# Performance work log

Hardware: AMD Instinct MI355X
Metric: run time of the kernel (lower is better)

The kernel has to match this reference:

```python
import jax, jax.numpy as jnp
import numpy as np

NUM_ITERATIONS = 5
BIG = 1e30


def _compute_cv(vc, Hf, norm):
    # vc: [B, M, N]; Hf: [M, N] float 0/1 mask; norm: scalar normalization factor
    # sign part: product of signs of incoming messages per check, redistributed
    sign_info = (1.0 - Hf)[None] + vc            # non-edges -> +1 so they don't affect the product
    s = jnp.sign(sign_info)
    row_sign = jnp.prod(s, axis=2, keepdims=True)  # [B, M, 1]
    result_sign = row_sign * Hf * s              # extrinsic sign per edge (self sign divided out)
    # magnitude part: min / second-min over edges of each check (masked top-2)
    back = jnp.where(Hf == 0.0, -BIG - 1.0, 0.0)[None]  # push non-edges to -inf-ish
    a = jnp.clip(jnp.abs(vc), 0.0, BIG)
    decision = -a + back                          # top-2 of this = two smallest magnitudes on edges
    top2 = jax.lax.top_k(decision, 2)[0]          # [B, M, 2]
    mn = (-top2[:, :, 0:1]) * Hf                  # smallest magnitude, broadcast on edges
    sub = (-top2[:, :, 1:2]) * Hf                 # second smallest
    res = jnp.where(a > mn, mn, sub)              # extrinsic min (exclude self if self is the min)
    return norm * res * jax.lax.stop_gradient(result_sign)


def setup_inputs() -> dict:
    key = jax.random.key(0)
    k1, k2, k3 = jax.random.split(key, 3)
    B, M, N = 16, 1024, 2048
    soft_input = jax.random.normal(k1, (B, N), dtype=jnp.float32) * 2.0
    # sparse binary parity-check matrix (Tanner graph), ~20 ones per row, min degree 2
    H = (jax.random.uniform(k2, (M, N)) < 0.01).astype(jnp.int32)
    H = H.at[:, :2].set(1)
    labels = jax.random.randint(k3, (B, N), 0, 2).astype(jnp.int32)
    w = jnp.full((1,), -0.048, dtype=jnp.float32)
    return {"soft_input": soft_input, "H": H, "labels": labels, "w": w}


def reference(soft_input, H, labels, w):
    Hf = H.astype(jnp.float32)
    norm = jax.nn.softplus(w)  # NMS-1 normalized factor, shape [1]
    soft_output = soft_input
    for _ in range(NUM_ITERATIONS):
        vc = soft_output[:, None, :] * Hf          # variable-to-check messages [B, M, N]
        cv = _compute_cv(vc, Hf, norm)             # check-to-variable messages [B, M, N]
        soft_output = soft_input + jnp.sum(cv, axis=1)  # marginalize
    return soft_output
```

## Files before the change

kernel.cpp:

```cpp
#include <hip/hip_runtime.h>

#define BB 16
#define MM 1024
#define NN 2048
#define RCAP 64
#define CCAP 48
#define INFF __builtin_inff()

typedef unsigned short u16;

__device__ __forceinline__ float signf(float x) {
    return (x > 0.0f) ? 1.0f : ((x < 0.0f) ? -1.0f : 0.0f);
}

__device__ __forceinline__ void mmerge(float& mn, float& sub, float om, float os) {
    float hi = fmaxf(mn, om);
    mn = fminf(mn, om);
    sub = fminf(fminf(sub, os), hi);
}

__global__ __launch_bounds__(256)
void build_stats1(const int4* __restrict__ H4, const float* __restrict__ soft_in,
                  int* __restrict__ row_deg, u16* __restrict__ row_cols,
                  int* __restrict__ col_deg, u16* __restrict__ col_rows,
                  float4* __restrict__ stats_out, const float* __restrict__ wptr) {
    __shared__ u16 s_cols[RCAP];
    __shared__ int s_cnt;
    const int m = blockIdx.x, t = threadIdx.x;
    if (t == 0) s_cnt = 0;
    __syncthreads();

    const int4* hrow = H4 + m * (NN / 4);
#pragma unroll
    for (int half = 0; half < 2; ++half) {
        int i = t + half * 256;
        int4 h = hrow[i];
        int hv[4] = {h.x, h.y, h.z, h.w};
#pragma unroll
        for (int k = 0; k < 4; ++k) {
            if (hv[k]) {
                int c = i * 4 + k;
                int j = atomicAdd(&s_cnt, 1);
                if (j < RCAP) s_cols[j] = (u16)c;
                if (c >= 2) {
                    int j2 = atomicAdd(&col_deg[c], 1);
                    if (j2 < CCAP) col_rows[c * CCAP + j2] = (u16)m;
                }
            }
        }
    }
    __syncthreads();
    const int deg = min(s_cnt, RCAP);
    if (t == 0) row_deg[m] = deg;
    if (t < 8) ((int4*)(row_cols + m * RCAP))[t] = ((const int4*)s_cols)[t];

    const int b = t >> 4, k = t & 15;
    const float norm = log1pf(expf(wptr[0]));
    const float* sp = soft_in + b * NN;
    float sgn = 1.0f, mn = INFF, sub = INFF;
    for (int j = k; j < deg; j += 16) {
        float x = sp[s_cols[j]];
        sgn *= signf(x);
        float a = fabsf(x);
        if (a < mn) { sub = mn; mn = a; }
        else if (a < sub) sub = a;
    }
#pragma unroll
    for (int off = 1; off < 16; off <<= 1) {
        sgn *= __shfl_xor(sgn, off, 16);
        float om = __shfl_xor(mn, off, 16);
        float os = __shfl_xor(sub, off, 16);
        mmerge(mn, sub, om, os);
    }
    if (k == 0) stats_out[b * MM + m] = make_float4(norm * sgn, mn, sub, 0.0f);
}

__global__ __launch_bounds__(64)
void phase_a(const float* __restrict__ soft,
             const int* __restrict__ row_deg, const u16* __restrict__ row_cols,
             float4* __restrict__ stats_out, const float* __restrict__ wptr) {
    const int blk = blockIdx.x;
    const int b = blk >> 4;
    const int m = ((blk & 15) << 6) + threadIdx.x;
    const float norm = log1pf(expf(wptr[0]));
    const float* sp = soft + b * NN;
    const int deg = row_deg[m];
    const int4* ip = (const int4*)(row_cols + m * RCAP);
    float sgn = 1.0f, mn = INFF, sub = INFF;
#pragma unroll
    for (int jb = 0; jb < RCAP; jb += 8) {
        if (jb < deg) {
            int4 iv = ip[jb >> 3];
            const u16* q = (const u16*)&iv;
#pragma unroll
            for (int k = 0; k < 8; ++k) {
                float x = sp[q[k] & (NN - 1)];
                x = (jb + k < deg) ? x : INFF;
                sgn *= signf(x);
                float a = fabsf(x);
                if (a < mn) { sub = mn; mn = a; }
                else if (a < sub) sub = a;
            }
        }
    }
    stats_out[b * MM + m] = make_float4(norm * sgn, mn, sub, 0.0f);
}

__global__ __launch_bounds__(64)
void phase_b(const float* __restrict__ soft_src, const float* __restrict__ soft_in,
             float* __restrict__ dst, const float4* __restrict__ stats,
             const int* __restrict__ col_deg, const u16* __restrict__ col_rows) {
    const int blk = blockIdx.x, t = threadIdx.x;
    if (blk < 512) {
        const int b = blk >> 5;
        const int n = ((blk & 31) << 6) + t;
        if (n < 2) return;
        const float4* st = stats + b * MM;
        float x = soft_src[b * NN + n];
        float a = fabsf(x), sx = signf(x), acc = 0.0f;
        const int deg = min(col_deg[n], CCAP);
        const int4* ip = (const int4*)(col_rows + n * CCAP);
#pragma unroll
        for (int jb = 0; jb < CCAP; jb += 8) {
            if (jb < deg) {
                int4 iv = ip[jb >> 3];
                const u16* q = (const u16*)&iv;
#pragma unroll
                for (int k = 0; k < 8; ++k) {
                    float4 s = st[q[k] & (MM - 1)];
                    float cv = s.x * ((a > s.y) ? s.y : s.z) * sx;
                    acc += (jb + k < deg) ? cv : 0.0f;
                }
            }
        }
        dst[b * NN + n] = soft_in[b * NN + n] + acc;
    } else {
        const int h = blk - 512;
        const int b = h >> 1, c = h & 1;
        const float4* st = stats + b * MM;
        float x = soft_src[b * NN + c];
        float a = fabsf(x), sx = signf(x), acc = 0.0f;
#pragma unroll
        for (int i = 0; i < 16; ++i) {
            float4 s = st[t + 64 * i];
            acc += s.x * ((a > s.y) ? s.y : s.z) * sx;
        }
#pragma unroll
        for (int off = 1; off < 64; off <<= 1) acc += __shfl_xor(acc, off);
        if (t == 0) dst[b * NN + c] = soft_in[b * NN + c] + acc;
    }
}

extern "C" void kernel_launch(void* const* d_in, const int* in_sizes, int n_in,
                              void* d_out, int out_size, void* d_ws, size_t ws_size,
                              hipStream_t stream) {
    const float* soft_in = (const float*)d_in[0];
    const int*   H       = (const int*)d_in[1];
    const float* w       = (const float*)d_in[3];
    float* out = (float*)d_out;

    char* ws = (char*)d_ws;
    int* col_deg  = (int*)ws;
    int* row_deg  = (int*)(ws + 8192);
    u16* row_cols = (u16*)(ws + 12288);
    u16* col_rows = (u16*)(ws + 143360);
    float4* statsA = (float4*)(ws + 339968);
    float4* statsB = (float4*)(ws + 602112);
    float* softX = (float*)(ws + 864256);
    float* softY = (float*)(ws + 995328);

    hipMemsetAsync(col_deg, 0, NN * sizeof(int), stream);
    build_stats1<<<MM, 256, 0, stream>>>((const int4*)H, soft_in, row_deg, row_cols,
                                         col_deg, col_rows, statsA, w);
    phase_b<<<544, 64, 0, stream>>>(soft_in, soft_in, softX, statsA, col_deg, col_rows);
    phase_a<<<256, 64, 0, stream>>>(softX, row_deg, row_cols, statsB, w);
    phase_b<<<544, 64, 0, stream>>>(softX, soft_in, softY, statsB, col_deg, col_rows);
    phase_a<<<256, 64, 0, stream>>>(softY, row_deg, row_cols, statsA, w);
    phase_b<<<544, 64, 0, stream>>>(softY, soft_in, softX, statsA, col_deg, col_rows);
    phase_a<<<256, 64, 0, stream>>>(softX, row_deg, row_cols, statsB, w);
    phase_b<<<544, 64, 0, stream>>>(softX, soft_in, softY, statsB, col_deg, col_rows);
    phase_a<<<256, 64, 0, stream>>>(softY, row_deg, row_cols, statsA, w);
    phase_b<<<544, 64, 0, stream>>>(softY, soft_in, out, statsA, col_deg, col_rows);
}
```

Measured before the change: 126.3 us.

## Build column adjacency with dedicated column-scan blocks instead of global atomics

Adds 128 extra blocks to the build kernel that each scan 16 columns of H directly, in 16 row segments, and assemble sorted column row-lists in shared memory. The per-edge global atomicAdd on col_deg and the scattered col_rows writes in the row blocks are removed, and so is the memset of col_deg. The cost is a second, strided read of H (column-wise, coalesced across the 16 columns) and a serial merge by 16 threads per block. It also makes the column lists deterministic and row-ordered.

```diff
diff --git a/kernel.cpp b/kernel.cpp
--- a/kernel.cpp
+++ b/kernel.cpp
@@ -20,13 +20,53 @@
 }
 
 __global__ __launch_bounds__(256)
-void build_stats1(const int4* __restrict__ H4, const float* __restrict__ soft_in,
+void build_stats1(const int4* __restrict__ H4, const int* __restrict__ H,
+                  const float* __restrict__ soft_in,
                   int* __restrict__ row_deg, u16* __restrict__ row_cols,
                   int* __restrict__ col_deg, u16* __restrict__ col_rows,
                   float4* __restrict__ stats_out, const float* __restrict__ wptr) {
+    const int t = threadIdx.x;
+
+    if (blockIdx.x >= MM) {
+        __shared__ u16 s_list[16 * 16 * 16];
+        __shared__ unsigned char s_c[256];
+        const int n0 = (blockIdx.x - MM) * 16;
+        const int cl = t & 15, seg = t >> 4;
+        const int n = n0 + cl;
+        const int r0 = seg * 64;
+        const int* p = H + r0 * NN + n;
+        int cnt = 0;
+        u16* lst = s_list + (cl * 16 + seg) * 16;
+        for (int base = 0; base < 64; base += 8) {
+            int v[8];
+#pragma unroll
+            for (int k = 0; k < 8; ++k) v[k] = p[(base + k) * NN];
+#pragma unroll
+            for (int k = 0; k < 8; ++k) {
+                if (v[k]) { if (cnt < 16) lst[cnt] = (u16)(r0 + base + k); ++cnt; }
+            }
+        }
+        s_c[t] = (unsigned char)min(cnt, 16);
+        __syncthreads();
+        if (t < 16) {
+            int pos = 0;
+            u16* dst = col_rows + (n0 + t) * CCAP;
+            for (int sg = 0; sg < 16; ++sg) {
+                const int c2 = s_c[sg * 16 + t];
+                const u16* sl = s_list + (t * 16 + sg) * 16;
+                for (int j = 0; j < c2; ++j) {
+                    if (pos < CCAP) dst[pos] = sl[j];
+                    ++pos;
+                }
+            }
+            col_deg[n0 + t] = min(pos, CCAP);
+        }
+        return;
+    }
+
     __shared__ u16 s_cols[RCAP];
     __shared__ int s_cnt;
-    const int m = blockIdx.x, t = threadIdx.x;
+    const int m = blockIdx.x;
     if (t == 0) s_cnt = 0;
     __syncthreads();
 
@@ -39,13 +79,8 @@
 #pragma unroll
         for (int k = 0; k < 4; ++k) {
             if (hv[k]) {
-                int c = i * 4 + k;
                 int j = atomicAdd(&s_cnt, 1);
-                if (j < RCAP) s_cols[j] = (u16)c;
-                if (c >= 2) {
-                    int j2 = atomicAdd(&col_deg[c], 1);
-                    if (j2 < CCAP) col_rows[c * CCAP + j2] = (u16)m;
-                }
+                if (j < RCAP) s_cols[j] = (u16)(i * 4 + k);
             }
         }
     }
@@ -160,8 +195,8 @@
     float* out = (float*)d_out;
 
     char* ws = (char*)d_ws;
-    int* col_deg  = (int*)ws;
-    int* row_deg  = (int*)(ws + 8192);
+    int* row_deg  = (int*)ws;
+    int* col_deg  = (int*)(ws + 4096);
     u16* row_cols = (u16*)(ws + 12288);
     u16* col_rows = (u16*)(ws + 143360);
     float4* statsA = (float4*)(ws + 339968);
@@ -169,9 +204,9 @@
     float* softX = (float*)(ws + 864256);
     float* softY = (float*)(ws + 995328);
 
-    hipMemsetAsync(col_deg, 0, NN * sizeof(int), stream);
-    build_stats1<<<MM, 256, 0, stream>>>((const int4*)H, soft_in, row_deg, row_cols,
-                                         col_deg, col_rows, statsA, w);
+    build_stats1<<<MM + 128, 256, 0, stream>>>((const int4*)H, H, soft_in,
+                                               row_deg, row_cols, col_deg, col_rows,
+                                               statsA, w);
     phase_b<<<544, 64, 0, stream>>>(soft_in, soft_in, softX, statsA, col_deg, col_rows);
     phase_a<<<256, 64, 0, stream>>>(softX, row_deg, row_cols, statsB, w);
     phase_b<<<544, 64, 0, stream>>>(softX, soft_in, softY, statsB, col_deg, col_rows);
```

After: 134.1 us. +6.2%, slower.
